# Performance work log

Measured on AMD Instinct MI355X. Metric: run time of the kernel, lower is better.

Reference implementation:

```python
import jax, jax.numpy as jnp
import numpy as np

N = 64        # SSM state size
L = 262144    # l_max / sequence length


def setup_inputs() -> dict:
    key = jax.random.key(0)
    ks = jax.random.split(key, 8)
    u = jax.random.normal(ks[0], (L,), dtype=jnp.float32)
    # HiPPO-DPLR style eigenvalue init
    Lambda_re = -0.5 * jnp.ones((N,), jnp.float32)
    Lambda_im = jnp.pi * jnp.arange(N, dtype=jnp.float32)
    P_re = jax.random.normal(ks[1], (N,), jnp.float32)
    P_im = jax.random.normal(ks[2], (N,), jnp.float32)
    B_re = jax.random.normal(ks[3], (N,), jnp.float32)
    B_im = jax.random.normal(ks[4], (N,), jnp.float32)
    C_ri = (0.5 ** 0.5) * jax.random.normal(ks[5], (N, 2), jnp.float32)  # C = C_ri[:,0] + i*C_ri[:,1]
    D = jnp.ones((1,), jnp.float32)
    log_step = jax.random.uniform(ks[6], (1,), jnp.float32,
                                  minval=float(np.log(0.001)), maxval=float(np.log(0.1)))
    return {"u": u, "Lambda_re": Lambda_re, "Lambda_im": Lambda_im,
            "P_re": P_re, "P_im": P_im, "B_re": B_re, "B_im": B_im,
            "C_ri": C_ri, "D": D, "log_step": log_step}


def _kernel_DPLR(Lambda, P, Q, B, C, step, l):
    # Evaluate the SSM generating function at the l roots of unity (bilinear discretization)
    Omega = jnp.exp((-2j * jnp.pi) * (jnp.arange(l) / l))          # (L,)
    g = (2.0 / step) * ((1.0 - Omega) / (1.0 + Omega))             # (L,)
    c = 2.0 / (1.0 + Omega)                                        # (L,)
    # Core Cauchy matrix: the single large (L, N) complex intermediate
    recip = 1.0 / (g[:, None] - Lambda[None, :])                   # (L, N)
    # Four Cauchy dot products fused into one thin matmul
    v = jnp.stack([C.conj() * B, C.conj() * P,
                   Q.conj() * B, Q.conj() * P], axis=1)            # (N, 4)
    k = recip @ v                                                  # (L, 4)
    k00, k01, k10, k11 = k[:, 0], k[:, 1], k[:, 2], k[:, 3]
    atRoots = c * (k00 - k01 * (1.0 / (1.0 + k11)) * k10)          # (L,)
    return jnp.fft.ifft(atRoots, l).real                           # (L,) real kernel


def _causal_convolution(u, K):
    l = u.shape[0]
    ud = jnp.fft.rfft(jnp.pad(u, (0, K.shape[0])))
    Kd = jnp.fft.rfft(jnp.pad(K, (0, l)))
    return jnp.fft.irfft(ud * Kd)[:l]


def reference(u, Lambda_re, Lambda_im, P_re, P_im, B_re, B_im, C_ri, D, log_step):
    Lambda = Lambda_re + 1j * Lambda_im
    P = P_re + 1j * P_im
    B = B_re + 1j * B_im
    C = C_ri[:, 0] + 1j * C_ri[:, 1]
    step = jnp.exp(log_step)                                       # (1,)
    K = _kernel_DPLR(Lambda, P, P, B, C, step, u.shape[0])
    return _causal_convolution(u, K) + D * u
```

## Files before the change

### kernel.cpp

```cpp
#include <hip/hip_runtime.h>
#include <math.h>

#define L_LEN  262144
#define NST    64
#define TPB    256
#define TSTR   544
#define PI2F   6.2831853071795864769f
#define PIF    3.1415926535897932385f

__device__ inline float2 cmul(float2 a, float2 b) {
    return make_float2(a.x*b.x - a.y*b.y, a.x*b.y + a.y*b.x);
}

template<int M, int NF>
__device__ float2* lds_fft_r4(float2* b0, float2* b1, float sgn) {
    float2* src = b0; float2* dst = b1;
    int Ns = 1;
    while (Ns * 4 <= M) {
        __syncthreads();
        const int NB = NF * (M / 4);
        for (int bi = threadIdx.x; bi < NB; bi += TPB) {
            int f = bi / (M / 4);
            int j = bi & (M / 4 - 1);
            int r = j & (Ns - 1);
            const float2* s = src + f * M;
            float2 x0 = s[j];
            float2 x1 = s[j +     (M/4)];
            float2 x2 = s[j + 2 * (M/4)];
            float2 x3 = s[j + 3 * (M/4)];
            float ang = sgn * PI2F * ((float)r / (float)(4 * Ns));
            float sn, cs; __sincosf(ang, &sn, &cs);
            float2 w1 = make_float2(cs, sn);
            float2 w2 = cmul(w1, w1);
            float2 w3 = cmul(w2, w1);
            x1 = cmul(x1, w1); x2 = cmul(x2, w2); x3 = cmul(x3, w3);
            float2 t0 = make_float2(x0.x + x2.x, x0.y + x2.y);
            float2 t1 = make_float2(x0.x - x2.x, x0.y - x2.y);
            float2 t2 = make_float2(x1.x + x3.x, x1.y + x3.y);
            float2 t3 = make_float2(x1.x - x3.x, x1.y - x3.y);
            float2* d = dst + f * M + ((j - r) << 2) + r;
            d[0]      = make_float2(t0.x + t2.x, t0.y + t2.y);
            d[Ns]     = make_float2(t1.x - sgn * t3.y, t1.y + sgn * t3.x);
            d[2 * Ns] = make_float2(t0.x - t2.x, t0.y - t2.y);
            d[3 * Ns] = make_float2(t1.x + sgn * t3.y, t1.y - sgn * t3.x);
        }
        float2* t = src; src = dst; dst = t;
        Ns <<= 2;
    }
    if (Ns < M) {
        __syncthreads();
        const int NB = NF * (M / 2);
        for (int bi = threadIdx.x; bi < NB; bi += TPB) {
            int f = bi / (M / 2);
            int j = bi & (M / 2 - 1);
            const float2* s = src + f * M;
            float2 a = s[j];
            float2 b = s[j + M / 2];
            float ang = sgn * PI2F * ((float)j / (float)M);
            float sn, cs; __sincosf(ang, &sn, &cs);
            float2 wb = make_float2(cs * b.x - sn * b.y, cs * b.y + sn * b.x);
            float2* d = dst + f * M + j;
            d[0]     = make_float2(a.x + wb.x, a.y + wb.y);
            d[M / 2] = make_float2(a.x - wb.x, a.y - wb.y);
        }
        float2* t = src; src = dst; dst = t;
    }
    __syncthreads();
    return src;
}


__global__ __launch_bounds__(TPB) void kI(
    const float* __restrict__ u,
    const float* __restrict__ Lre, const float* __restrict__ Lim,
    const float* __restrict__ Pre, const float* __restrict__ Pim,
    const float* __restrict__ Bre, const float* __restrict__ Bim,
    const float* __restrict__ Cri, const float* __restrict__ lstp,
    float2* __restrict__ Acm, float2* __restrict__ T_K,
    float2* __restrict__ T_U, float2* __restrict__ T_Uo)
{
    __shared__ float2 b0[2048], b1[2048];
    __shared__ float4 cA[NST], cB[NST], cC[NST], cD[NST];
    const int t = threadIdx.x, bx = blockIdx.x;
    const int c0 = (bx & 255) << 1;
    const float invL = 1.0f / (float)L_LEN;
    if (bx < 256) {
        if (t < NST) {
            float lr = Lre[t], li = Lim[t];
            float pr = Pre[t], pi = Pim[t];
            float br = Bre[t], bi = Bim[t];
            float cr = Cri[2*t], ci = Cri[2*t+1];
            float dx = -lr;
            float v00x = cr*br + ci*bi, v00y = cr*bi - ci*br;
            float v01x = cr*pr + ci*pi, v01y = cr*pi - ci*pr;
            float v10x = pr*br + pi*bi, v10y = pr*bi - pi*br;
            float v11x = pr*pr + pi*pi;
            cA[t] = make_float4(li, dx*dx, dx*v11x, -v11x);
            cB[t] = make_float4(dx*v00x, v00y, dx*v00y, -v00x);
            cC[t] = make_float4(dx*v01x, v01y, dx*v01y, -v01x);
            cD[t] = make_float4(dx*v10x, v10y, dx*v10y, -v10x);
        }
        __syncthreads();
        float G2 = 2.0f / expf(lstp[0]);
        float tn[4], gi[4], acc[4][8];
        #pragma unroll
        for (int p = 0; p < 4; ++p) {
            int i = t + (p << 8);
            int f = i >> 9, e = i & 511;
            int m = (c0 + f) + (e << 9);
            float h = PIF * ((float)m * invL);
            float sn, cs; __sincosf(h, &sn, &cs);
            float tv = sn * __frcp_rn(cs);
            tv = fminf(fmaxf(tv, -1e7f), 1e7f);
            tn[p] = tv; gi[p] = G2 * tv;
            #pragma unroll
            for (int q = 0; q < 8; ++q) acc[p][q] = 0.f;
        }
        #pragma unroll 2
        for (int n = 0; n < NST; ++n) {
            float4 a = cA[n], b = cB[n], cc = cC[n], d = cD[n];
            #pragma unroll
            for (int p = 0; p < 4; ++p) {
                float dy   = gi[p] - a.x;
                float iv   = __frcp_rn(fmaf(dy, dy, a.y));
                float ivdy = iv * dy;
                acc[p][6] = fmaf(iv, a.z, acc[p][6]);
                acc[p][7] = fmaf(ivdy, a.w, acc[p][7]);
                acc[p][0] = fmaf(iv, b.x,  fmaf(ivdy, b.y,  acc[p][0]));
                acc[p][1] = fmaf(iv, b.z,  fmaf(ivdy, b.w,  acc[p][1]));
                acc[p][2] = fmaf(iv, cc.x, fmaf(ivdy, cc.y, acc[p][2]));
                acc[p][3] = fmaf(iv, cc.z, fmaf(ivdy, cc.w, acc[p][3]));
                acc[p][4] = fmaf(iv, d.x,  fmaf(ivdy, d.y,  acc[p][4]));
                acc[p][5] = fmaf(iv, d.z,  fmaf(ivdy, d.w,  acc[p][5]));
            }
        }
        #pragma unroll
        for (int p = 0; p < 4; ++p) {
            int i = t + (p << 8);
            int f = i >> 9, e = i & 511;
            float ax = 1.f + acc[p][6], ay = acc[p][7];
            float im = 1.f / (ax*ax + ay*ay);
            float tx = acc[p][2]*acc[p][4] - acc[p][3]*acc[p][5];
            float ty = acc[p][2]*acc[p][5] + acc[p][3]*acc[p][4];
            float wx = acc[p][0] - (tx*ax + ty*ay) * im;
            float wy = acc[p][1] - (ty*ax - tx*ay) * im;
            float2 A = make_float2(wx - tn[p]*wy, wy + tn[p]*wx);
            Acm[((c0 + f) << 9) + e] = A;
            b0[i] = A;
        }
        float2* r = lds_fft_r4<512, 2>(b0, b1, +1.f);
        for (int i = t; i < 1024; i += TPB) {
            int f = i & 1, k = i >> 1;
            int c = c0 + f;
            float ang = PI2F * ((float)(c * k) * invL);
            float sn, cs; __sincosf(ang, &sn, &cs);
            T_K[k * TSTR + c] = cmul(make_float2(cs, sn), r[(f << 9) + k]);
        }
    } else {
        for (int i = t; i < 1024; i += TPB) {
            int f = i & 1, e = i >> 1;
            int n = (c0 + f) + (e << 9);
            float uv = u[n];
            float sn, cs; __sincosf(PIF * ((float)n * invL), &sn, &cs);
            b0[(f << 9) + e]       = make_float2(uv, 0.f);
            b0[((2 + f) << 9) + e] = make_float2(uv * cs, -uv * sn);
        }
        float2* r = lds_fft_r4<512, 4>(b0, b1, -1.f);
        for (int i = t; i < 2048; i += TPB) {
            int f = i & 1, k = (i >> 1) & 511, v = i >> 10;
            int c = c0 + f;
            float ang = -PI2F * ((float)(c * k) * invL);
            float sn, cs; __sincosf(ang, &sn, &cs);
            float2 val = cmul(make_float2(cs, sn), r[(((v << 1) + f) << 9) + k]);
            if (v == 0) T_U [k * TSTR + c] = val;
            else        T_Uo[k * TSTR + c] = val;
        }
    }
}

__global__ __launch_bounds__(TPB) void kII(
    const float2* __restrict__ T_K, const float2* __restrict__ T_U,
    const float2* __restrict__ T_Uo,
    float2* __restrict__ T_Ko, float2* __restrict__ Ue, float2* __restrict__ Uo)
{
    __shared__ float2 b0[2048], b1[2048];
    const int t = threadIdx.x, bx = blockIdx.x;
    const int c0 = (bx & 255) << 1;
    const float invL = 1.0f / (float)L_LEN;
    if (bx < 256) {
        for (int i = t; i < 1024; i += TPB)
            b0[i] = T_K[(c0 + (i >> 9)) * TSTR + (i & 511)];
        float2* r = lds_fft_r4<512, 2>(b0, b1, +1.f);
        float2* o = (r == b0) ? b1 : b0;
        for (int i = t; i < 1024; i += TPB) {
            int f = i >> 9, o1 = i & 511;
            int n = (c0 + f) + (o1 << 9);
            float K = r[i].x * invL;
            float sn, cs; __sincosf(PIF * ((float)n * invL), &sn, &cs);
            o[i] = make_float2(K * cs, -K * sn);
        }
        float2* r2 = lds_fft_r4<512, 2>(o, r, -1.f);
        for (int i = t; i < 1024; i += TPB) {
            int f = i & 1, k = i >> 1;
            int c = c0 + f;
            float ang = -PI2F * ((float)(c * k) * invL);
            float sn, cs; __sincosf(ang, &sn, &cs);
            T_Ko[k * TSTR + c] = cmul(make_float2(cs, sn), r2[(f << 9) + k]);
        }
    } else {
        for (int i = t; i < 2048; i += TPB) {
            int v = i >> 10, f = (i >> 9) & 1, e = i & 511;
            const float2* Tin = v ? T_Uo : T_U;
            b0[i] = Tin[(c0 + f) * TSTR + e];
        }
        float2* r = lds_fft_r4<512, 4>(b0, b1, -1.f);
        for (int i = t; i < 2048; i += TPB) {
            int v = i >> 10, f = (i >> 9) & 1, k2 = i & 511;
            float2* Xo = v ? Uo : Ue;
            Xo[((c0 + f) << 9) + k2] = r[i];
        }
    }
}

__global__ __launch_bounds__(TPB) void kIII(
    const float2* __restrict__ T_Ko, const float2* __restrict__ Ue,
    const float2* __restrict__ Uo, const float2* __restrict__ Acm,
    float2* __restrict__ T_Ve, float2* __restrict__ T_Vo)
{
    __shared__ float2 b0[1024], b1[1024];
    const int t = threadIdx.x, kc = blockIdx.x;
    const float invL = 1.0f / (float)L_LEN;
    for (int i = t; i < 512; i += TPB)
        b0[i] = T_Ko[kc * TSTR + i];
    float2* r = lds_fft_r4<512, 1>(b0, b1, -1.f);
    float2* o = (r == b0) ? b1 : b0;
    for (int i = t; i < 512; i += TPB) {
        float2 ko = r[i];
        float2 ue = Ue [(kc << 9) + i];
        float2 uo = Uo [(kc << 9) + i];
        float2 av = Acm[(kc << 9) + i];
        o[i]       = cmul(ue, av);
        o[i + 512] = cmul(uo, ko);
    }
    float2* r2 = lds_fft_r4<512, 2>(o, r, +1.f);
    for (int i = t; i < 1024; i += TPB) {
        int v = i >> 9, k = i & 511;
        float ang = PI2F * ((float)(kc * k) * invL);
        float sn, cs; __sincosf(ang, &sn, &cs);
        float2 val = cmul(make_float2(cs, sn), r2[(v << 9) + k]);
        if (v == 0) T_Ve[k * TSTR + kc] = val;
        else        T_Vo[k * TSTR + kc] = val;
    }
}

__global__ __launch_bounds__(TPB) void kIV(
    const float2* __restrict__ T_Ve, const float2* __restrict__ T_Vo,
    const float* __restrict__ u, const float* __restrict__ Dp,
    float* __restrict__ out)
{
    __shared__ float2 b0[1024], b1[1024];
    const int t = threadIdx.x, k = blockIdx.x;
    const float invL = 1.0f / (float)L_LEN;
    for (int i = t; i < 512; i += TPB) {
        b0[i]       = T_Ve[k * TSTR + i];
        b0[i + 512] = T_Vo[k * TSTR + i];
    }
    float2* r = lds_fft_r4<512, 2>(b0, b1, +1.f);
    const float sc = 0.5f * invL;
    const float D = Dp[0];
    for (int o1 = t; o1 < 512; o1 += TPB) {
        int n = k + (o1 << 9);
        float sn, cs; __sincosf(PIF * ((float)n * invL), &sn, &cs);
        float2 yE = r[o1];
        float2 yO = r[o1 + 512];
        out[n] = fmaf(D, u[n], (yE.x + cs * yO.x - sn * yO.y) * sc);
    }
}

extern "C" void kernel_launch(void* const* d_in, const int* in_sizes, int n_in,
                              void* d_out, int out_size, void* d_ws, size_t ws_size,
                              hipStream_t stream) {
    const float* u    = (const float*)d_in[0];
    const float* Lre  = (const float*)d_in[1];
    const float* Lim  = (const float*)d_in[2];
    const float* Pre  = (const float*)d_in[3];
    const float* Pim  = (const float*)d_in[4];
    const float* Bre  = (const float*)d_in[5];
    const float* Bim  = (const float*)d_in[6];
    const float* Cri  = (const float*)d_in[7];
    const float* Dp   = (const float*)d_in[8];
    const float* lstp = (const float*)d_in[9];
    float* out = (float*)d_out;

    char* ws = (char*)d_ws;
    float2* Acm  = (float2*)(ws);
    float2* Ue   = (float2*)(ws + 0x200000);
    float2* Uo   = (float2*)(ws + 0x400000);
    float2* T_K  = (float2*)(ws + 0x600000);
    float2* T_U  = (float2*)(ws + 0x820000);
    float2* T_Uo = (float2*)(ws + 0xA40000);
    float2* T_Ko = (float2*)(ws + 0xC60000);
    float2* T_Ve = (float2*)(ws + 0xE80000);
    float2* T_Vo = (float2*)(ws + 0x10A0000);

    kI  <<<512, TPB, 0, stream>>>(u, Lre,Lim,Pre,Pim,Bre,Bim,Cri,lstp,
                                  Acm, T_K, T_U, T_Uo);
    kII <<<512, TPB, 0, stream>>>(T_K, T_U, T_Uo, T_Ko, Ue, Uo);
    kIII<<<512, TPB, 0, stream>>>(T_Ko, Ue, Uo, Acm, T_Ve, T_Vo);
    kIV <<<512, TPB, 0, stream>>>(T_Ve, T_Vo, u, Dp, out);
}
```

Measured before the change: 117.2 us.

## Fuse four FFT-stage kernels into one cooperative kernel with grid syncs

Merges the four separate kernel launches into one cooperative kernel of 512 blocks, with grid.sync() between stages. Each block now handles one column and does both the Cauchy/kernel work and the input FFT, instead of splitting those roles across block halves. Global loads for the next stage are prefetched before the LDS FFTs, and the correctly-rounded reciprocals are replaced by the raw hardware rcp. The aim is to remove launch gaps and tail imbalance between kernels. In exchange it relies on grid-wide barriers and co-residency of all blocks, and gives up some rcp precision.

```diff
diff --git a/kernel.cpp b/kernel.cpp
--- a/kernel.cpp
+++ b/kernel.cpp
@@ -1,9 +1,13 @@
 #include <hip/hip_runtime.h>
+#include <hip/hip_cooperative_groups.h>
 #include <math.h>
+
+namespace cg = cooperative_groups;
 
 #define L_LEN  262144
 #define NST    64
 #define TPB    256
+#define NBLK   512
 #define TSTR   544
 #define PI2F   6.2831853071795864769f
 #define PIF    3.1415926535897932385f
@@ -11,6 +15,7 @@
 __device__ inline float2 cmul(float2 a, float2 b) {
     return make_float2(a.x*b.x - a.y*b.y, a.x*b.y + a.y*b.x);
 }
+__device__ inline float frcp(float x) { return __builtin_amdgcn_rcpf(x); }
 
 template<int M, int NF>
 __device__ float2* lds_fft_r4(float2* b0, float2* b1, float sgn) {
@@ -69,48 +74,51 @@
     return src;
 }
 
-
-__global__ __launch_bounds__(TPB) void kI(
+__global__ __launch_bounds__(TPB, 2) void fused(
     const float* __restrict__ u,
     const float* __restrict__ Lre, const float* __restrict__ Lim,
     const float* __restrict__ Pre, const float* __restrict__ Pim,
     const float* __restrict__ Bre, const float* __restrict__ Bim,
     const float* __restrict__ Cri, const float* __restrict__ lstp,
+    const float* __restrict__ Dp, float* __restrict__ out,
     float2* __restrict__ Acm, float2* __restrict__ T_K,
-    float2* __restrict__ T_U, float2* __restrict__ T_Uo)
+    float2* __restrict__ T_U, float2* __restrict__ T_Uo,
+    float2* __restrict__ T_Ko, float2* __restrict__ Ue, float2* __restrict__ Uo,
+    float2* __restrict__ T_Ve, float2* __restrict__ T_Vo)
 {
-    __shared__ float2 b0[2048], b1[2048];
+    __shared__ float2 b0[1024], b1[1024];
     __shared__ float4 cA[NST], cB[NST], cC[NST], cD[NST];
-    const int t = threadIdx.x, bx = blockIdx.x;
-    const int c0 = (bx & 255) << 1;
+    cg::grid_group grid = cg::this_grid();
+    const int t = threadIdx.x;
+    const int c = blockIdx.x;
     const float invL = 1.0f / (float)L_LEN;
-    if (bx < 256) {
-        if (t < NST) {
-            float lr = Lre[t], li = Lim[t];
-            float pr = Pre[t], pi = Pim[t];
-            float br = Bre[t], bi = Bim[t];
-            float cr = Cri[2*t], ci = Cri[2*t+1];
-            float dx = -lr;
-            float v00x = cr*br + ci*bi, v00y = cr*bi - ci*br;
-            float v01x = cr*pr + ci*pi, v01y = cr*pi - ci*pr;
-            float v10x = pr*br + pi*bi, v10y = pr*bi - pi*br;
-            float v11x = pr*pr + pi*pi;
-            cA[t] = make_float4(li, dx*dx, dx*v11x, -v11x);
-            cB[t] = make_float4(dx*v00x, v00y, dx*v00y, -v00x);
-            cC[t] = make_float4(dx*v01x, v01y, dx*v01y, -v01x);
-            cD[t] = make_float4(dx*v10x, v10y, dx*v10y, -v10x);
-        }
-        __syncthreads();
+
+    if (t < NST) {
+        float lr = Lre[t], li = Lim[t];
+        float pr = Pre[t], pi = Pim[t];
+        float br = Bre[t], bi = Bim[t];
+        float cr = Cri[2*t], ci = Cri[2*t+1];
+        float dx = -lr;
+        float v00x = cr*br + ci*bi, v00y = cr*bi - ci*br;
+        float v01x = cr*pr + ci*pi, v01y = cr*pi - ci*pr;
+        float v10x = pr*br + pi*bi, v10y = pr*bi - pi*br;
+        float v11x = pr*pr + pi*pi;
+        cA[t] = make_float4(li, dx*dx, dx*v11x, -v11x);
+        cB[t] = make_float4(dx*v00x, v00y, dx*v00y, -v00x);
+        cC[t] = make_float4(dx*v01x, v01y, dx*v01y, -v01x);
+        cD[t] = make_float4(dx*v10x, v10y, dx*v10y, -v10x);
+    }
+    __syncthreads();
+    {
         float G2 = 2.0f / expf(lstp[0]);
-        float tn[4], gi[4], acc[4][8];
+        float tn[2], gi[2], acc[2][8];
         #pragma unroll
-        for (int p = 0; p < 4; ++p) {
-            int i = t + (p << 8);
-            int f = i >> 9, e = i & 511;
-            int m = (c0 + f) + (e << 9);
+        for (int p = 0; p < 2; ++p) {
+            int e = t + (p << 8);
+            int m = c + (e << 9);
             float h = PIF * ((float)m * invL);
             float sn, cs; __sincosf(h, &sn, &cs);
-            float tv = sn * __frcp_rn(cs);
+            float tv = sn * frcp(cs);
             tv = fminf(fmaxf(tv, -1e7f), 1e7f);
             tn[p] = tv; gi[p] = G2 * tv;
             #pragma unroll
@@ -120,9 +128,9 @@
         for (int n = 0; n < NST; ++n) {
             float4 a = cA[n], b = cB[n], cc = cC[n], d = cD[n];
             #pragma unroll
-            for (int p = 0; p < 4; ++p) {
+            for (int p = 0; p < 2; ++p) {
                 float dy   = gi[p] - a.x;
-                float iv   = __frcp_rn(fmaf(dy, dy, a.y));
+                float iv   = frcp(fmaf(dy, dy, a.y));
                 float ivdy = iv * dy;
                 acc[p][6] = fmaf(iv, a.z, acc[p][6]);
                 acc[p][7] = fmaf(ivdy, a.w, acc[p][7]);
@@ -134,146 +142,126 @@
                 acc[p][5] = fmaf(iv, d.z,  fmaf(ivdy, d.w,  acc[p][5]));
             }
         }
+        float uv0 = u[c + (t << 9)];
+        float uv1 = u[c + ((t + 256) << 9)];
         #pragma unroll
-        for (int p = 0; p < 4; ++p) {
-            int i = t + (p << 8);
-            int f = i >> 9, e = i & 511;
+        for (int p = 0; p < 2; ++p) {
+            int e = t + (p << 8);
             float ax = 1.f + acc[p][6], ay = acc[p][7];
-            float im = 1.f / (ax*ax + ay*ay);
+            float im = frcp(ax*ax + ay*ay);
             float tx = acc[p][2]*acc[p][4] - acc[p][3]*acc[p][5];
             float ty = acc[p][2]*acc[p][5] + acc[p][3]*acc[p][4];
             float wx = acc[p][0] - (tx*ax + ty*ay) * im;
             float wy = acc[p][1] - (ty*ax - tx*ay) * im;
             float2 A = make_float2(wx - tn[p]*wy, wy + tn[p]*wx);
-            Acm[((c0 + f) << 9) + e] = A;
-            b0[i] = A;
-        }
-        float2* r = lds_fft_r4<512, 2>(b0, b1, +1.f);
+            Acm[(c << 9) + e] = A;
+            b0[e] = A;
+        }
+        float2* rA = lds_fft_r4<512, 1>(b0, b1, +1.f);
+        for (int k = t; k < 512; k += TPB) {
+            float ang = PI2F * ((float)(c * k) * invL);
+            float sn, cs; __sincosf(ang, &sn, &cs);
+            T_K[k * TSTR + c] = cmul(make_float2(cs, sn), rA[k]);
+        }
+        __syncthreads();
+        {
+            int n0 = c + (t << 9), n1 = c + ((t + 256) << 9);
+            float sn, cs;
+            __sincosf(PIF * ((float)n0 * invL), &sn, &cs);
+            b0[t]        = make_float2(uv0, 0.f);
+            b0[512 + t]  = make_float2(uv0 * cs, -uv0 * sn);
+            __sincosf(PIF * ((float)n1 * invL), &sn, &cs);
+            b0[t + 256]       = make_float2(uv1, 0.f);
+            b0[512 + t + 256] = make_float2(uv1 * cs, -uv1 * sn);
+        }
+        float2* rU = lds_fft_r4<512, 2>(b0, b1, -1.f);
         for (int i = t; i < 1024; i += TPB) {
-            int f = i & 1, k = i >> 1;
-            int c = c0 + f;
-            float ang = PI2F * ((float)(c * k) * invL);
-            float sn, cs; __sincosf(ang, &sn, &cs);
-            T_K[k * TSTR + c] = cmul(make_float2(cs, sn), r[(f << 9) + k]);
-        }
-    } else {
-        for (int i = t; i < 1024; i += TPB) {
-            int f = i & 1, e = i >> 1;
-            int n = (c0 + f) + (e << 9);
-            float uv = u[n];
-            float sn, cs; __sincosf(PIF * ((float)n * invL), &sn, &cs);
-            b0[(f << 9) + e]       = make_float2(uv, 0.f);
-            b0[((2 + f) << 9) + e] = make_float2(uv * cs, -uv * sn);
-        }
-        float2* r = lds_fft_r4<512, 4>(b0, b1, -1.f);
-        for (int i = t; i < 2048; i += TPB) {
-            int f = i & 1, k = (i >> 1) & 511, v = i >> 10;
-            int c = c0 + f;
+            int v = i >> 9, k = i & 511;
             float ang = -PI2F * ((float)(c * k) * invL);
             float sn, cs; __sincosf(ang, &sn, &cs);
-            float2 val = cmul(make_float2(cs, sn), r[(((v << 1) + f) << 9) + k]);
+            float2 val = cmul(make_float2(cs, sn), rU[(v << 9) + k]);
             if (v == 0) T_U [k * TSTR + c] = val;
             else        T_Uo[k * TSTR + c] = val;
         }
     }
-}
-
-__global__ __launch_bounds__(TPB) void kII(
-    const float2* __restrict__ T_K, const float2* __restrict__ T_U,
-    const float2* __restrict__ T_Uo,
-    float2* __restrict__ T_Ko, float2* __restrict__ Ue, float2* __restrict__ Uo)
-{
-    __shared__ float2 b0[2048], b1[2048];
-    const int t = threadIdx.x, bx = blockIdx.x;
-    const int c0 = (bx & 255) << 1;
-    const float invL = 1.0f / (float)L_LEN;
-    if (bx < 256) {
-        for (int i = t; i < 1024; i += TPB)
-            b0[i] = T_K[(c0 + (i >> 9)) * TSTR + (i & 511)];
-        float2* r = lds_fft_r4<512, 2>(b0, b1, +1.f);
-        float2* o = (r == b0) ? b1 : b0;
-        for (int i = t; i < 1024; i += TPB) {
-            int f = i >> 9, o1 = i & 511;
-            int n = (c0 + f) + (o1 << 9);
-            float K = r[i].x * invL;
+    grid.sync();
+
+    {
+        float2 pu0 = T_U [c * TSTR + t];
+        float2 pu1 = T_U [c * TSTR + t + 256];
+        float2 po0 = T_Uo[c * TSTR + t];
+        float2 po1 = T_Uo[c * TSTR + t + 256];
+        for (int i = t; i < 512; i += TPB) b0[i] = T_K[c * TSTR + i];
+        float2* rK = lds_fft_r4<512, 1>(b0, b1, +1.f);
+        float2* o = (rK == b0) ? b1 : b0;
+        for (int i = t; i < 512; i += TPB) {
+            int n = c + (i << 9);
+            float K = rK[i].x * invL;
             float sn, cs; __sincosf(PIF * ((float)n * invL), &sn, &cs);
             o[i] = make_float2(K * cs, -K * sn);
         }
-        float2* r2 = lds_fft_r4<512, 2>(o, r, -1.f);
+        float2* r2 = lds_fft_r4<512, 1>(o, rK, -1.f);
+        for (int k = t; k < 512; k += TPB) {
+            float ang = -PI2F * ((float)(c * k) * invL);
+            float sn, cs; __sincosf(ang, &sn, &cs);
+            T_Ko[k * TSTR + c] = cmul(make_float2(cs, sn), r2[k]);
+        }
+        __syncthreads();
+        b0[t]             = pu0;
+        b0[t + 256]       = pu1;
+        b0[512 + t]       = po0;
+        b0[512 + t + 256] = po1;
+        float2* rUU = lds_fft_r4<512, 2>(b0, b1, -1.f);
         for (int i = t; i < 1024; i += TPB) {
-            int f = i & 1, k = i >> 1;
-            int c = c0 + f;
-            float ang = -PI2F * ((float)(c * k) * invL);
-            float sn, cs; __sincosf(ang, &sn, &cs);
-            T_Ko[k * TSTR + c] = cmul(make_float2(cs, sn), r2[(f << 9) + k]);
-        }
-    } else {
-        for (int i = t; i < 2048; i += TPB) {
-            int v = i >> 10, f = (i >> 9) & 1, e = i & 511;
-            const float2* Tin = v ? T_Uo : T_U;
-            b0[i] = Tin[(c0 + f) * TSTR + e];
-        }
-        float2* r = lds_fft_r4<512, 4>(b0, b1, -1.f);
-        for (int i = t; i < 2048; i += TPB) {
-            int v = i >> 10, f = (i >> 9) & 1, k2 = i & 511;
-            float2* Xo = v ? Uo : Ue;
-            Xo[((c0 + f) << 9) + k2] = r[i];
-        }
-    }
-}
-
-__global__ __launch_bounds__(TPB) void kIII(
-    const float2* __restrict__ T_Ko, const float2* __restrict__ Ue,
-    const float2* __restrict__ Uo, const float2* __restrict__ Acm,
-    float2* __restrict__ T_Ve, float2* __restrict__ T_Vo)
-{
-    __shared__ float2 b0[1024], b1[1024];
-    const int t = threadIdx.x, kc = blockIdx.x;
-    const float invL = 1.0f / (float)L_LEN;
-    for (int i = t; i < 512; i += TPB)
-        b0[i] = T_Ko[kc * TSTR + i];
-    float2* r = lds_fft_r4<512, 1>(b0, b1, -1.f);
-    float2* o = (r == b0) ? b1 : b0;
-    for (int i = t; i < 512; i += TPB) {
-        float2 ko = r[i];
-        float2 ue = Ue [(kc << 9) + i];
-        float2 uo = Uo [(kc << 9) + i];
-        float2 av = Acm[(kc << 9) + i];
-        o[i]       = cmul(ue, av);
-        o[i + 512] = cmul(uo, ko);
-    }
-    float2* r2 = lds_fft_r4<512, 2>(o, r, +1.f);
-    for (int i = t; i < 1024; i += TPB) {
-        int v = i >> 9, k = i & 511;
-        float ang = PI2F * ((float)(kc * k) * invL);
-        float sn, cs; __sincosf(ang, &sn, &cs);
-        float2 val = cmul(make_float2(cs, sn), r2[(v << 9) + k]);
-        if (v == 0) T_Ve[k * TSTR + kc] = val;
-        else        T_Vo[k * TSTR + kc] = val;
-    }
-}
-
-__global__ __launch_bounds__(TPB) void kIV(
-    const float2* __restrict__ T_Ve, const float2* __restrict__ T_Vo,
-    const float* __restrict__ u, const float* __restrict__ Dp,
-    float* __restrict__ out)
-{
-    __shared__ float2 b0[1024], b1[1024];
-    const int t = threadIdx.x, k = blockIdx.x;
-    const float invL = 1.0f / (float)L_LEN;
-    for (int i = t; i < 512; i += TPB) {
-        b0[i]       = T_Ve[k * TSTR + i];
-        b0[i + 512] = T_Vo[k * TSTR + i];
-    }
-    float2* r = lds_fft_r4<512, 2>(b0, b1, +1.f);
-    const float sc = 0.5f * invL;
-    const float D = Dp[0];
-    for (int o1 = t; o1 < 512; o1 += TPB) {
-        int n = k + (o1 << 9);
-        float sn, cs; __sincosf(PIF * ((float)n * invL), &sn, &cs);
-        float2 yE = r[o1];
-        float2 yO = r[o1 + 512];
-        out[n] = fmaf(D, u[n], (yE.x + cs * yO.x - sn * yO.y) * sc);
+            int v = i >> 9, k2 = i & 511;
+            (v ? Uo : Ue)[(c << 9) + k2] = rUU[i];
+        }
+    }
+    grid.sync();
+
+    {
+        float2 qe0 = Ue [(c << 9) + t],  qe1 = Ue [(c << 9) + t + 256];
+        float2 qo0 = Uo [(c << 9) + t],  qo1 = Uo [(c << 9) + t + 256];
+        float2 qa0 = Acm[(c << 9) + t],  qa1 = Acm[(c << 9) + t + 256];
+        for (int i = t; i < 512; i += TPB) b0[i] = T_Ko[c * TSTR + i];
+        float2* rKo = lds_fft_r4<512, 1>(b0, b1, -1.f);
+        float2* o3 = (rKo == b0) ? b1 : b0;
+        o3[t]             = cmul(qe0, qa0);
+        o3[t + 256]       = cmul(qe1, qa1);
+        o3[512 + t]       = cmul(qo0, rKo[t]);
+        o3[512 + t + 256] = cmul(qo1, rKo[t + 256]);
+        float2* rV = lds_fft_r4<512, 2>(o3, rKo, +1.f);
+        for (int i = t; i < 1024; i += TPB) {
+            int v = i >> 9, k = i & 511;
+            float ang = PI2F * ((float)(c * k) * invL);
+            float sn, cs; __sincosf(ang, &sn, &cs);
+            float2 val = cmul(make_float2(cs, sn), rV[(v << 9) + k]);
+            if (v == 0) T_Ve[k * TSTR + c] = val;
+            else        T_Vo[k * TSTR + c] = val;
+        }
+    }
+    grid.sync();
+
+    {
+        float un0 = u[c + (t << 9)];
+        float un1 = u[c + ((t + 256) << 9)];
+        const float D = Dp[0];
+        for (int i = t; i < 512; i += TPB) {
+            b0[i]       = T_Ve[c * TSTR + i];
+            b0[i + 512] = T_Vo[c * TSTR + i];
+        }
+        float2* rY = lds_fft_r4<512, 2>(b0, b1, +1.f);
+        const float sc = 0.5f * invL;
+        #pragma unroll
+        for (int p = 0; p < 2; ++p) {
+            int o1 = t + (p << 8);
+            int n = c + (o1 << 9);
+            float sn, cs; __sincosf(PIF * ((float)n * invL), &sn, &cs);
+            float2 yE = rY[o1];
+            float2 yO = rY[o1 + 512];
+            float uv = p ? un1 : un0;
+            out[n] = fmaf(D, uv, (yE.x + cs * yO.x - sn * yO.y) * sc);
+        }
     }
 }
 
@@ -303,9 +291,13 @@
     float2* T_Ve = (float2*)(ws + 0xE80000);
     float2* T_Vo = (float2*)(ws + 0x10A0000);
 
-    kI  <<<512, TPB, 0, stream>>>(u, Lre,Lim,Pre,Pim,Bre,Bim,Cri,lstp,
-                                  Acm, T_K, T_U, T_Uo);
-    kII <<<512, TPB, 0, stream>>>(T_K, T_U, T_Uo, T_Ko, Ue, Uo);
-    kIII<<<512, TPB, 0, stream>>>(T_Ko, Ue, Uo, Acm, T_Ve, T_Vo);
-    kIV <<<512, TPB, 0, stream>>>(T_Ve, T_Vo, u, Dp, out);
+    void* args[] = {
+        (void*)&u, (void*)&Lre, (void*)&Lim, (void*)&Pre, (void*)&Pim,
+        (void*)&Bre, (void*)&Bim, (void*)&Cri, (void*)&lstp, (void*)&Dp,
+        (void*)&out,
+        (void*)&Acm, (void*)&T_K, (void*)&T_U, (void*)&T_Uo,
+        (void*)&T_Ko, (void*)&Ue, (void*)&Uo, (void*)&T_Ve, (void*)&T_Vo
+    };
+    hipLaunchCooperativeKernel(reinterpret_cast<void*>(fused),
+                               dim3(NBLK), dim3(TPB), args, 0, stream);
 }
```

New measurement: 315.3 us. 2.69x slower.
